# Optimization experiments

Measured on AMD Instinct MI355X. Metric: run time of the kernel, lower is better.

Reference implementation:

```python
import jax, jax.numpy as jnp
import numpy as np

N = 2048      # num_nodes (padded graph size)
D = 128       # node_embedding_dim
E = 8         # edge_embedding_dim (num learned edge-type channels)
ITERS = 8     # GGNN iterations (shared weights)


def setup_inputs() -> dict:
    key = jax.random.key(0)
    ks = jax.random.split(key, 8)
    s = 1.0 / np.sqrt(D)
    return {
        "node_embeddings": jax.random.normal(ks[0], (N, D), jnp.float32),
        # dense edge tensor; scaled by 1/N so the sum-over-senders message
        # aggregation stays O(1) in magnitude (real graphs are sparse)
        "edge_embeddings": jax.random.uniform(ks[1], (N, N, E), jnp.float32) / N,
        "W_msg": jax.random.normal(ks[2], (E, D, D), jnp.float32) * s,
        "b_msg": jnp.zeros((D,), jnp.float32),
        "Wi": jax.random.normal(ks[3], (D, 3 * D), jnp.float32) * s,
        "Wh": jax.random.normal(ks[4], (D, 3 * D), jnp.float32) * s,
        "b_gru": jnp.zeros((3 * D,), jnp.float32),
        "A_readout": jax.random.normal(ks[5], (D, D), jnp.float32) * s,
    }


def reference(node_embeddings, edge_embeddings, W_msg, b_msg, Wi, Wh, b_gru, A_readout):
    """GGNN steps (LinearMessagePassing + GRU update, weights shared via scan)
    followed by pairwise bilinear edge readout -> [N, N] logits."""

    def step(h, _):
        # per-edge-type linear transform of sender embeddings: [N, E, D]
        per_edge = jnp.einsum('sd,edh->seh', h, W_msg)
        # aggregate over senders weighted by dense edge tensor: [N, D]
        messages = jnp.einsum('ste,seh->th', edge_embeddings, per_edge) + b_msg
        # gated recurrent (GRU) update: state = node embeddings, input = messages
        gi = messages @ Wi + b_gru            # [N, 3D]
        gh = h @ Wh                           # [N, 3D]
        i_r, i_z, i_n = jnp.split(gi, 3, axis=-1)
        h_r, h_z, h_n = jnp.split(gh, 3, axis=-1)
        r = jax.nn.sigmoid(i_r + h_r)
        z = jax.nn.sigmoid(i_z + h_z)
        n = jnp.tanh(i_n + r * h_n)
        h_new = (1.0 - z) * n + z * h
        return h_new, None

    h, _ = jax.lax.scan(step, node_embeddings, None, length=ITERS)
    # bilinear pairwise readout -> weighted adjacency logits [N, N]
    logits = jnp.einsum('id,de,je->ij', h, A_readout, h)
    return logits
```

## Files before the change

### kernel.cpp

```cpp
#include <hip/hip_runtime.h>
#include <math.h>
#include <stdint.h>

#define Nn 2048
#define Dd 128
#define Ee 8
#define NIT 8
#define KT (Nn*Ee)
#define KSPLIT 32

typedef __bf16 bf16;
typedef __attribute__((ext_vector_type(8))) __bf16 bf16x8;
typedef __attribute__((ext_vector_type(4))) __bf16 bf16x4;
typedef __attribute__((ext_vector_type(4))) float f32x4;
typedef __attribute__((ext_vector_type(16))) float f32x16;

__device__ __forceinline__ f32x4 mfma16(bf16x8 a, bf16x8 b, f32x4 c){
    return __builtin_amdgcn_mfma_f32_16x16x32_bf16(a, b, c, 0, 0, 0);
}
__device__ __forceinline__ f32x16 mfma32(bf16x8 a, bf16x8 b, f32x16 c){
    return __builtin_amdgcn_mfma_f32_32x32x16_bf16(a, b, c, 0, 0, 0);
}
__device__ __forceinline__ void g2lds16(const void* g, void* l){
    __builtin_amdgcn_global_load_lds((const uint32_t*)g, (uint32_t*)l, 16, 0, 0);
}

__global__ __launch_bounds__(256) void k_prep(
    const float* __restrict__ node, const float* __restrict__ Wmsg,
    const float* __restrict__ Wi,   const float* __restrict__ Wh,
    const float* __restrict__ Ar,
    float* __restrict__ h32, bf16* __restrict__ hb,
    bf16* __restrict__ WmT, bf16* __restrict__ WiT, bf16* __restrict__ WhT,
    bf16* __restrict__ ArT)
{
    int tid = blockIdx.x*256 + threadIdx.x;
    int stride = gridDim.x*256;
    for (int i = tid; i < Nn*Dd; i += stride){
        float v = node[i]; h32[i] = v; hb[i] = (bf16)v;
    }
    for (int i = tid; i < Ee*Dd*Dd; i += stride){
        int e = i >> 14; int r = i & 16383; int h = r >> 7; int d = r & 127;
        WmT[i] = (bf16)Wmsg[e*Dd*Dd + d*Dd + h];
    }
    for (int i = tid; i < 384*Dd; i += stride){
        int j = i >> 7; int d = i & 127;
        WiT[i] = (bf16)Wi[d*384 + j];
        WhT[i] = (bf16)Wh[d*384 + j];
    }
    for (int i = tid; i < Dd*Dd; i += stride){
        int h = i >> 7; int d = i & 127;
        ArT[i] = (bf16)Ar[d*Dd + h];
    }
}

__global__ __launch_bounds__(256) void k_per_edge(
    const bf16* __restrict__ hb, const bf16* __restrict__ WmT,
    bf16* __restrict__ Pt)
{
    __shared__ bf16 Blds[Ee][16][Dd+8];
    const int s0 = blockIdx.x * 64;
    const int h0 = blockIdx.y * 16;
    const int tid = threadIdx.x;
    for (int i = 0; i < 8; i++){
        int idx = tid + i*256;
        int e = idx >> 8, row = (idx >> 4) & 15, c = idx & 15;
        *(bf16x8*)&Blds[e][row][c*8] =
            *(const bf16x8*)&WmT[e*Dd*Dd + (h0+row)*Dd + c*8];
    }
    __syncthreads();
    const int lane = tid & 63, wave = tid >> 6;
    const int quad = lane >> 4, l16 = lane & 15;
    const int srow = s0 + wave*16 + l16;
    f32x4 acc[Ee];
    for (int e = 0; e < Ee; e++) acc[e] = (f32x4){0.f,0.f,0.f,0.f};
    for (int kk = 0; kk < 4; kk++){
        int k0 = kk*32 + quad*8;
        bf16x8 a = *(const bf16x8*)&hb[srow*Dd + k0];
        for (int e = 0; e < Ee; e++){
            bf16x8 b = *(const bf16x8*)&Blds[e][l16][k0];
            acc[e] = mfma16(a, b, acc[e]);
        }
    }
    const int h = h0 + l16;
    for (int r = 0; r < 4; r++){
        int s = s0 + wave*16 + quad*4 + r;
        bf16x8 po;
        for (int e = 0; e < Ee; e++) po[e] = (bf16)acc[e][r];
        *(bf16x8*)&Pt[((size_t)s*Dd + h)*Ee] = po;
    }
}

template<int FIRST>
__global__ __launch_bounds__(256) void k_msg_gemm(
    const float* __restrict__ edge_f, bf16* __restrict__ edge_bf,
    const bf16* __restrict__ Pt, bf16* __restrict__ msgP)
{
    __shared__ __align__(16) char ldsb[65536];
    const int flat = blockIdx.y*32 + blockIdx.x;
    const int kgroup = (flat & 7)*4 + ((flat >> 3) & 3);
    const int tgroup = flat >> 5;
    const int t0 = tgroup * 128;
    const int sblk = kgroup * 64;
    const int tid = threadIdx.x;
    const int lane = tid & 63, wave = tid >> 6;
    const int half = lane >> 5, l31 = lane & 31;
    const int trow = t0 + wave*32 + l31;
    const char* Ptb = (const char*)Pt;

    f32x16 acc[4];
    #pragma unroll
    for (int nt = 0; nt < 4; nt++)
        for (int i = 0; i < 16; i++) acc[nt][i] = 0.f;

    bf16x8 A0[8], A1[8];

#define STAGE(ch_) do{                                                         \
    const char* _src = Ptb + (size_t)(sblk + (ch_)*16)*2048                    \
                           + wave*1024 + lane*16;                              \
    char* _dst = ldsb + ((ch_)&1)*32768 + wave*1024;                           \
    _Pragma("unroll")                                                          \
    for (int j = 0; j < 8; j++)                                                \
        g2lds16(_src + j*4096, _dst + j*4096);                                 \
}while(0)

#define PREF(AD_, ch_) do{                                                     \
    int _sc = sblk + (ch_)*16 + half;                                          \
    _Pragma("unroll")                                                          \
    for (int ks = 0; ks < 8; ks++){                                            \
        size_t _off = (size_t)(_sc + ks*2)*16384 + trow*8;                     \
        if (FIRST){                                                            \
            f32x4 _v0 = *(const f32x4*)&edge_f[_off];                          \
            f32x4 _v1 = *(const f32x4*)&edge_f[_off+4];                        \
            bf16x8 _o;                                                         \
            for (int _j = 0; _j < 4; _j++){                                    \
                _o[_j] = (bf16)_v0[_j]; _o[_j+4] = (bf16)_v1[_j];              \
            }                                                                  \
            AD_[ks] = _o;                                                      \
            *(bf16x8*)&edge_bf[_off] = _o;                                     \
        } else {                                                               \
            AD_[ks] = *(const bf16x8*)&edge_bf[_off];                          \
        }                                                                      \
    }                                                                          \
}while(0)

#define COMPUTE(AD_, ch_) do{                                                  \
    const bf16* _bt = (const bf16*)(ldsb + ((ch_)&1)*32768);                   \
    _Pragma("unroll")                                                          \
    for (int ks = 0; ks < 8; ks++){                                            \
        const bf16* _bp = _bt + (ks*2 + half)*1024 + l31*8;                    \
        acc[0] = mfma32(AD_[ks], *(const bf16x8*)(_bp      ), acc[0]);         \
        acc[1] = mfma32(AD_[ks], *(const bf16x8*)(_bp + 256), acc[1]);         \
        acc[2] = mfma32(AD_[ks], *(const bf16x8*)(_bp + 512), acc[2]);         \
        acc[3] = mfma32(AD_[ks], *(const bf16x8*)(_bp + 768), acc[3]);         \
    }                                                                          \
}while(0)

    STAGE(0); PREF(A0, 0);
    asm volatile("s_waitcnt vmcnt(0)" ::: "memory");
    __syncthreads();
    #pragma unroll
    for (int cc = 0; cc < 2; cc++){
        const int ch = cc*2;
        STAGE(ch+1); PREF(A1, ch+1);
        COMPUTE(A0, ch);
        asm volatile("s_waitcnt vmcnt(0)" ::: "memory");
        __syncthreads();
        if (ch+2 < 4){ STAGE(ch+2); PREF(A0, ch+2); }
        COMPUTE(A1, ch+1);
        if (ch+2 < 4){
            asm volatile("s_waitcnt vmcnt(0)" ::: "memory");
            __syncthreads();
        }
    }
#undef STAGE
#undef PREF
#undef COMPUTE

    bf16* dst = msgP + (size_t)kgroup*(Nn*Dd);
    #pragma unroll
    for (int nt = 0; nt < 4; nt++){
        int h = nt*32 + l31;
        #pragma unroll
        for (int r = 0; r < 16; r++){
            int row = (r&3) + 8*(r>>2) + 4*half;
            dst[(size_t)(t0 + wave*32 + row)*Dd + h] = (bf16)acc[nt][r];
        }
    }
}

__global__ __launch_bounds__(256) void k_msg_reduce(
    const bf16* __restrict__ msgP, const float* __restrict__ bmsg,
    bf16* __restrict__ msgb)
{
    const int base = (blockIdx.x*256 + threadIdx.x)*4;
    const int d0 = base & (Dd-1);
    f32x4 s = *(const f32x4*)&bmsg[d0];
    #pragma unroll
    for (int p = 0; p < KSPLIT; p++){
        bf16x4 v = *(const bf16x4*)&msgP[(size_t)p*Nn*Dd + base];
        #pragma unroll
        for (int j = 0; j < 4; j++) s[j] += (float)v[j];
    }
    bf16x4 o;
    #pragma unroll
    for (int j = 0; j < 4; j++) o[j] = (bf16)s[j];
    *(bf16x4*)&msgb[base] = o;
}

__global__ __launch_bounds__(256) void k_gru(
    const bf16* __restrict__ msgb, const bf16* __restrict__ WiT,
    const bf16* __restrict__ WhT, const float* __restrict__ bgru,
    float* __restrict__ h32, bf16* __restrict__ hb)
{
    __shared__ __align__(16) bf16 stage[384][40];
    __shared__ float Gs[16][384];
    __shared__ float Ghn[16][128];

    const int t0 = blockIdx.x * 16;
    const int tid = threadIdx.x;
    const int lane = tid & 63, wave = tid >> 6;
    const int quad = lane >> 4, l16 = lane & 15;

    f32x4 accA[6], accB[6];
    for (int i = 0; i < 6; i++){ accA[i] = (f32x4){0.f,0.f,0.f,0.f}; accB[i] = (f32x4){0.f,0.f,0.f,0.f}; }

    for (int mat = 0; mat < 2; mat++){
        const bf16* WT = mat == 0 ? WiT : WhT;
        for (int kc = 0; kc < 4; kc++){
            for (int i = 0; i < 6; i++){
                int idx = tid + i*256; int row = idx >> 2, c = idx & 3;
                *(bf16x8*)&stage[row][c*8] = *(const bf16x8*)&WT[row*Dd + kc*32 + c*8];
            }
            __syncthreads();
            int k0 = kc*32 + quad*8;
            bf16x8 a;
            if (mat == 0) a = *(const bf16x8*)&msgb[(t0 + l16)*Dd + k0];
            else          a = *(const bf16x8*)&hb  [(t0 + l16)*Dd + k0];
            for (int tt = 0; tt < 6; tt++){
                int T = wave*6 + tt;
                bf16x8 b = *(const bf16x8*)&stage[T*16 + l16][quad*8];
                if (mat == 0 || T < 16) accA[tt] = mfma16(a, b, accA[tt]);
                else                    accB[tt] = mfma16(a, b, accB[tt]);
            }
            __syncthreads();
        }
    }
    for (int tt = 0; tt < 6; tt++){
        int T = wave*6 + tt;
        int j = T*16 + l16;
        for (int r = 0; r < 4; r++){
            int m = quad*4 + r;
            Gs[m][j] = accA[tt][r];
            if (T >= 16) Ghn[m][j - 256] = accB[tt][r];
        }
    }
    __syncthreads();
    for (int i = 0; i < 8; i++){
        int cell = tid + i*256;
        int m = cell >> 7, jd = cell & 127;
        int t = t0 + m;
        float xr = Gs[m][jd]       + bgru[jd];
        float xz = Gs[m][jd + 128] + bgru[jd + 128];
        float xn = Gs[m][jd + 256] + bgru[jd + 256];
        float r = 1.f / (1.f + expf(-xr));
        float z = 1.f / (1.f + expf(-xz));
        float n = tanhf(xn + r * Ghn[m][jd]);
        float ho = h32[t*Dd + jd];
        float hnew = (1.f - z) * n + z * ho;
        h32[t*Dd + jd] = hnew;
        hb [t*Dd + jd] = (bf16)hnew;
    }
}

__global__ __launch_bounds__(256) void k_read1(
    const bf16* __restrict__ hb, const bf16* __restrict__ ArT, bf16* __restrict__ t1)
{
    __shared__ bf16 Blds[Dd][Dd+8];
    const int s0 = blockIdx.x * 64;
    const int tid = threadIdx.x;
    for (int i = 0; i < 8; i++){
        int idx = tid + i*256; int row = idx >> 4, c = idx & 15;
        *(bf16x8*)&Blds[row][c*8] = *(const bf16x8*)&ArT[row*Dd + c*8];
    }
    __syncthreads();
    const int lane = tid & 63, wave = tid >> 6;
    const int quad = lane >> 4, l16 = lane & 15;
    const int srow = s0 + wave*16 + l16;
    f32x4 acc[8];
    for (int nt = 0; nt < 8; nt++) acc[nt] = (f32x4){0.f,0.f,0.f,0.f};
    for (int kk = 0; kk < 4; kk++){
        int k0 = kk*32 + quad*8;
        bf16x8 a = *(const bf16x8*)&hb[srow*Dd + k0];
        for (int nt = 0; nt < 8; nt++){
            bf16x8 b = *(const bf16x8*)&Blds[nt*16 + l16][k0];
            acc[nt] = mfma16(a, b, acc[nt]);
        }
    }
    for (int nt = 0; nt < 8; nt++){
        int h = nt*16 + l16;
        for (int r = 0; r < 4; r++){
            int s = s0 + wave*16 + quad*4 + r;
            t1[s*Dd + h] = (bf16)acc[nt][r];
        }
    }
}

__global__ __launch_bounds__(256) void k_read2(
    const bf16* __restrict__ t1, const bf16* __restrict__ hb, float* __restrict__ out)
{
    const int i0 = blockIdx.x * 64, j0 = blockIdx.y * 128;
    const int tid = threadIdx.x;
    const int lane = tid & 63, wave = tid >> 6;
    const int quad = lane >> 4, l16 = lane & 15;
    const int irow = i0 + wave*16 + l16;
    f32x4 acc[8];
    for (int nt = 0; nt < 8; nt++) acc[nt] = (f32x4){0.f,0.f,0.f,0.f};
    for (int kk = 0; kk < 4; kk++){
        int k0 = kk*32 + quad*8;
        bf16x8 a = *(const bf16x8*)&t1[irow*Dd + k0];
        for (int nt = 0; nt < 8; nt++){
            int j = j0 + nt*16 + l16;
            bf16x8 b = *(const bf16x8*)&hb[j*Dd + k0];
            acc[nt] = mfma16(a, b, acc[nt]);
        }
    }
    for (int nt = 0; nt < 8; nt++){
        int j = j0 + nt*16 + l16;
        for (int r = 0; r < 4; r++){
            int irw = i0 + wave*16 + quad*4 + r;
            out[(size_t)irw*Nn + j] = acc[nt][r];
        }
    }
}

extern "C" void kernel_launch(void* const* d_in, const int* in_sizes, int n_in,
                              void* d_out, int out_size, void* d_ws, size_t ws_size,
                              hipStream_t stream)
{
    const float* node = (const float*)d_in[0];
    const float* edge = (const float*)d_in[1];
    const float* Wmsg = (const float*)d_in[2];
    const float* bmsg = (const float*)d_in[3];
    const float* Wi   = (const float*)d_in[4];
    const float* Wh   = (const float*)d_in[5];
    const float* bgru = (const float*)d_in[6];
    const float* Ar   = (const float*)d_in[7];
    float* out = (float*)d_out;

    char* ws = (char*)d_ws;
    bf16*  edge_bf = (bf16*)ws;          ws += (size_t)Nn*Nn*Ee*2;
    bf16*  msgP = (bf16*)ws;             ws += (size_t)KSPLIT*Nn*Dd*2;
    bf16*  Pt  = (bf16*)ws;              ws += (size_t)Dd*KT*2;
    float* h32 = (float*)ws;             ws += (size_t)Nn*Dd*4;
    bf16*  hb  = (bf16*)ws;              ws += (size_t)Nn*Dd*2;
    bf16*  WmT = (bf16*)ws;              ws += (size_t)Ee*Dd*Dd*2;
    bf16*  WiT = (bf16*)ws;              ws += (size_t)384*Dd*2;
    bf16*  WhT = (bf16*)ws;              ws += (size_t)384*Dd*2;
    bf16*  ArT = (bf16*)ws;              ws += (size_t)Dd*Dd*2;
    bf16*  t1  = (bf16*)ws;              ws += (size_t)Nn*Dd*2;
    bf16*  msgb = t1;

    k_prep<<<dim3(256), 256, 0, stream>>>(node, Wmsg, Wi, Wh, Ar,
                                          h32, hb, WmT, WiT, WhT, ArT);
    for (int it = 0; it < NIT; it++){
        k_per_edge<<<dim3(32, 8), 256, 0, stream>>>(hb, WmT, Pt);
        if (it == 0)
            k_msg_gemm<1><<<dim3(32,16), 256, 0, stream>>>(edge, edge_bf, Pt, msgP);
        else
            k_msg_gemm<0><<<dim3(32,16), 256, 0, stream>>>(edge, edge_bf, Pt, msgP);
        k_msg_reduce<<<dim3(256), 256, 0, stream>>>(msgP, bmsg, msgb);
        k_gru<<<dim3(128), 256, 0, stream>>>(msgb, WiT, WhT, bgru, h32, hb);
    }
    k_read1<<<dim3(32),     256, 0, stream>>>(hb, ArT, t1);
    k_read2<<<dim3(32, 16), 256, 0, stream>>>(t1, hb, out);
}
```

Measured before the change: 561.0 us.

## Fuse message reduce and per-edge transform into GRU kernel; fuse readout GEMMs

```diff
diff --git a/kernel.cpp b/kernel.cpp
--- a/kernel.cpp
+++ b/kernel.cpp
@@ -188,38 +188,43 @@
     }
 }
 
-__global__ __launch_bounds__(256) void k_msg_reduce(
+__global__ __launch_bounds__(256) void k_gru2(
     const bf16* __restrict__ msgP, const float* __restrict__ bmsg,
-    bf16* __restrict__ msgb)
-{
-    const int base = (blockIdx.x*256 + threadIdx.x)*4;
-    const int d0 = base & (Dd-1);
-    f32x4 s = *(const f32x4*)&bmsg[d0];
-    #pragma unroll
-    for (int p = 0; p < KSPLIT; p++){
-        bf16x4 v = *(const bf16x4*)&msgP[(size_t)p*Nn*Dd + base];
-        #pragma unroll
-        for (int j = 0; j < 4; j++) s[j] += (float)v[j];
-    }
-    bf16x4 o;
-    #pragma unroll
-    for (int j = 0; j < 4; j++) o[j] = (bf16)s[j];
-    *(bf16x4*)&msgb[base] = o;
-}
-
-__global__ __launch_bounds__(256) void k_gru(
-    const bf16* __restrict__ msgb, const bf16* __restrict__ WiT,
-    const bf16* __restrict__ WhT, const float* __restrict__ bgru,
-    float* __restrict__ h32, bf16* __restrict__ hb)
+    const bf16* __restrict__ WiT,  const bf16* __restrict__ WhT,
+    const float* __restrict__ bgru, const bf16* __restrict__ WmT,
+    float* __restrict__ h32, bf16* __restrict__ hb, bf16* __restrict__ Pt)
 {
     __shared__ __align__(16) bf16 stage[384][40];
     __shared__ float Gs[16][384];
     __shared__ float Ghn[16][128];
+    __shared__ __align__(16) bf16 msg_b[16][136];
+    __shared__ __align__(16) bf16 hn_b[16][136];
 
     const int t0 = blockIdx.x * 16;
     const int tid = threadIdx.x;
     const int lane = tid & 63, wave = tid >> 6;
     const int quad = lane >> 4, l16 = lane & 15;
+
+    {
+        int m = tid >> 4;
+        int d0 = (tid & 15) * 8;
+        f32x4 s0 = *(const f32x4*)&bmsg[d0];
+        f32x4 s1 = *(const f32x4*)&bmsg[d0+4];
+        #pragma unroll
+        for (int p = 0; p < KSPLIT; p++){
+            bf16x8 v = *(const bf16x8*)&msgP[(size_t)p*Nn*Dd + (t0+m)*Dd + d0];
+            #pragma unroll
+            for (int j = 0; j < 4; j++){
+                s0[j] += (float)v[j];
+                s1[j] += (float)v[j+4];
+            }
+        }
+        bf16x8 o;
+        #pragma unroll
+        for (int j = 0; j < 4; j++){ o[j] = (bf16)s0[j]; o[j+4] = (bf16)s1[j]; }
+        *(bf16x8*)&msg_b[m][d0] = o;
+    }
+    __syncthreads();
 
     f32x4 accA[6], accB[6];
     for (int i = 0; i < 6; i++){ accA[i] = (f32x4){0.f,0.f,0.f,0.f}; accB[i] = (f32x4){0.f,0.f,0.f,0.f}; }
@@ -234,8 +239,8 @@
             __syncthreads();
             int k0 = kc*32 + quad*8;
             bf16x8 a;
-            if (mat == 0) a = *(const bf16x8*)&msgb[(t0 + l16)*Dd + k0];
-            else          a = *(const bf16x8*)&hb  [(t0 + l16)*Dd + k0];
+            if (mat == 0) a = *(const bf16x8*)&msg_b[l16][k0];
+            else          a = *(const bf16x8*)&hb[(t0 + l16)*Dd + k0];
             for (int tt = 0; tt < 6; tt++){
                 int T = wave*6 + tt;
                 bf16x8 b = *(const bf16x8*)&stage[T*16 + l16][quad*8];
@@ -255,6 +260,7 @@
         }
     }
     __syncthreads();
+
     for (int i = 0; i < 8; i++){
         int cell = tid + i*256;
         int m = cell >> 7, jd = cell & 127;
@@ -268,15 +274,52 @@
         float ho = h32[t*Dd + jd];
         float hnew = (1.f - z) * n + z * ho;
         h32[t*Dd + jd] = hnew;
-        hb [t*Dd + jd] = (bf16)hnew;
-    }
-}
-
-__global__ __launch_bounds__(256) void k_read1(
-    const bf16* __restrict__ hb, const bf16* __restrict__ ArT, bf16* __restrict__ t1)
+        bf16 hv = (bf16)hnew;
+        hb [t*Dd + jd] = hv;
+        hn_b[m][jd] = hv;
+    }
+    __syncthreads();
+
+    {
+        f32x4 accP[2][8];
+        #pragma unroll
+        for (int i = 0; i < 2; i++)
+            for (int e = 0; e < 8; e++) accP[i][e] = (f32x4){0.f,0.f,0.f,0.f};
+        #pragma unroll
+        for (int kk = 0; kk < 4; kk++){
+            int k0 = kk*32 + quad*8;
+            bf16x8 a = *(const bf16x8*)&hn_b[l16][k0];
+            #pragma unroll
+            for (int i = 0; i < 2; i++){
+                int th = wave*2 + i;
+                #pragma unroll
+                for (int e = 0; e < 8; e++){
+                    bf16x8 b = *(const bf16x8*)&WmT[e*Dd*Dd + (th*16 + l16)*Dd + k0];
+                    accP[i][e] = mfma16(a, b, accP[i][e]);
+                }
+            }
+        }
+        #pragma unroll
+        for (int i = 0; i < 2; i++){
+            int h = (wave*2 + i)*16 + l16;
+            #pragma unroll
+            for (int r = 0; r < 4; r++){
+                int s = quad*4 + r;
+                bf16x8 po;
+                for (int e = 0; e < 8; e++) po[e] = (bf16)accP[i][e][r];
+                *(bf16x8*)&Pt[((size_t)(t0 + s)*Dd + h)*Ee] = po;
+            }
+        }
+    }
+}
+
+__global__ __launch_bounds__(256) void k_read2f(
+    const bf16* __restrict__ hb, const bf16* __restrict__ ArT,
+    float* __restrict__ out)
 {
     __shared__ bf16 Blds[Dd][Dd+8];
-    const int s0 = blockIdx.x * 64;
+    __shared__ bf16 t1s[64][136];
+    const int i0 = blockIdx.x * 64, j0 = blockIdx.y * 128;
     const int tid = threadIdx.x;
     for (int i = 0; i < 8; i++){
         int idx = tid + i*256; int row = idx >> 4, c = idx & 15;
@@ -285,39 +328,34 @@
     __syncthreads();
     const int lane = tid & 63, wave = tid >> 6;
     const int quad = lane >> 4, l16 = lane & 15;
-    const int srow = s0 + wave*16 + l16;
+
+    {
+        const int srow = i0 + wave*16 + l16;
+        f32x4 acc1[8];
+        for (int nt = 0; nt < 8; nt++) acc1[nt] = (f32x4){0.f,0.f,0.f,0.f};
+        for (int kk = 0; kk < 4; kk++){
+            int k0 = kk*32 + quad*8;
+            bf16x8 a = *(const bf16x8*)&hb[srow*Dd + k0];
+            for (int nt = 0; nt < 8; nt++){
+                bf16x8 b = *(const bf16x8*)&Blds[nt*16 + l16][k0];
+                acc1[nt] = mfma16(a, b, acc1[nt]);
+            }
+        }
+        for (int nt = 0; nt < 8; nt++){
+            int h = nt*16 + l16;
+            for (int r = 0; r < 4; r++){
+                int rr = wave*16 + quad*4 + r;
+                t1s[rr][h] = (bf16)acc1[nt][r];
+            }
+        }
+    }
+    __syncthreads();
+
     f32x4 acc[8];
     for (int nt = 0; nt < 8; nt++) acc[nt] = (f32x4){0.f,0.f,0.f,0.f};
     for (int kk = 0; kk < 4; kk++){
         int k0 = kk*32 + quad*8;
-        bf16x8 a = *(const bf16x8*)&hb[srow*Dd + k0];
-        for (int nt = 0; nt < 8; nt++){
-            bf16x8 b = *(const bf16x8*)&Blds[nt*16 + l16][k0];
-            acc[nt] = mfma16(a, b, acc[nt]);
-        }
-    }
-    for (int nt = 0; nt < 8; nt++){
-        int h = nt*16 + l16;
-        for (int r = 0; r < 4; r++){
-            int s = s0 + wave*16 + quad*4 + r;
-            t1[s*Dd + h] = (bf16)acc[nt][r];
-        }
-    }
-}
-
-__global__ __launch_bounds__(256) void k_read2(
-    const bf16* __restrict__ t1, const bf16* __restrict__ hb, float* __restrict__ out)
-{
-    const int i0 = blockIdx.x * 64, j0 = blockIdx.y * 128;
-    const int tid = threadIdx.x;
-    const int lane = tid & 63, wave = tid >> 6;
-    const int quad = lane >> 4, l16 = lane & 15;
-    const int irow = i0 + wave*16 + l16;
-    f32x4 acc[8];
-    for (int nt = 0; nt < 8; nt++) acc[nt] = (f32x4){0.f,0.f,0.f,0.f};
-    for (int kk = 0; kk < 4; kk++){
-        int k0 = kk*32 + quad*8;
-        bf16x8 a = *(const bf16x8*)&t1[irow*Dd + k0];
+        bf16x8 a = *(const bf16x8*)&t1s[wave*16 + l16][k0];
         for (int nt = 0; nt < 8; nt++){
             int j = j0 + nt*16 + l16;
             bf16x8 b = *(const bf16x8*)&hb[j*Dd + k0];
@@ -357,20 +395,17 @@
     bf16*  WiT = (bf16*)ws;              ws += (size_t)384*Dd*2;
     bf16*  WhT = (bf16*)ws;              ws += (size_t)384*Dd*2;
     bf16*  ArT = (bf16*)ws;              ws += (size_t)Dd*Dd*2;
-    bf16*  t1  = (bf16*)ws;              ws += (size_t)Nn*Dd*2;
-    bf16*  msgb = t1;
 
     k_prep<<<dim3(256), 256, 0, stream>>>(node, Wmsg, Wi, Wh, Ar,
                                           h32, hb, WmT, WiT, WhT, ArT);
+    k_per_edge<<<dim3(32, 8), 256, 0, stream>>>(hb, WmT, Pt);
     for (int it = 0; it < NIT; it++){
-        k_per_edge<<<dim3(32, 8), 256, 0, stream>>>(hb, WmT, Pt);
         if (it == 0)
             k_msg_gemm<1><<<dim3(32,16), 256, 0, stream>>>(edge, edge_bf, Pt, msgP);
         else
             k_msg_gemm<0><<<dim3(32,16), 256, 0, stream>>>(edge, edge_bf, Pt, msgP);
-        k_msg_reduce<<<dim3(256), 256, 0, stream>>>(msgP, bmsg, msgb);
-        k_gru<<<dim3(128), 256, 0, stream>>>(msgb, WiT, WhT, bgru, h32, hb);
-    }
-    k_read1<<<dim3(32),     256, 0, stream>>>(hb, ArT, t1);
-    k_read2<<<dim3(32, 16), 256, 0, stream>>>(t1, hb, out);
-}
+        k_gru2<<<dim3(128), 256, 0, stream>>>(msgP, bmsg, WiT, WhT, bgru,
+                                              WmT, h32, hb, Pt);
+    }
+    k_read2f<<<dim3(32, 16), 256, 0, stream>>>(hb, ArT, out);
+}
```

After: 581.7 us. 1.04x slower.

## Fuse split-K message reduction into GRU kernel with 8-row tiles

Applied to the files above, without the earlier changes.

```diff
diff --git a/kernel.cpp b/kernel.cpp
--- a/kernel.cpp
+++ b/kernel.cpp
@@ -188,83 +188,87 @@
     }
 }
 
-__global__ __launch_bounds__(256) void k_msg_reduce(
+__global__ __launch_bounds__(256) void k_gru3(
     const bf16* __restrict__ msgP, const float* __restrict__ bmsg,
-    bf16* __restrict__ msgb)
-{
-    const int base = (blockIdx.x*256 + threadIdx.x)*4;
-    const int d0 = base & (Dd-1);
-    f32x4 s = *(const f32x4*)&bmsg[d0];
-    #pragma unroll
-    for (int p = 0; p < KSPLIT; p++){
-        bf16x4 v = *(const bf16x4*)&msgP[(size_t)p*Nn*Dd + base];
-        #pragma unroll
-        for (int j = 0; j < 4; j++) s[j] += (float)v[j];
-    }
-    bf16x4 o;
-    #pragma unroll
-    for (int j = 0; j < 4; j++) o[j] = (bf16)s[j];
-    *(bf16x4*)&msgb[base] = o;
-}
-
-__global__ __launch_bounds__(256) void k_gru(
-    const bf16* __restrict__ msgb, const bf16* __restrict__ WiT,
-    const bf16* __restrict__ WhT, const float* __restrict__ bgru,
+    const bf16* __restrict__ WiT, const bf16* __restrict__ WhT,
+    const float* __restrict__ bgru,
     float* __restrict__ h32, bf16* __restrict__ hb)
 {
-    __shared__ __align__(16) bf16 stage[384][40];
-    __shared__ float Gs[16][384];
-    __shared__ float Ghn[16][128];
-
-    const int t0 = blockIdx.x * 16;
+    __shared__ __align__(16) bf16 msg_b[16][136];
+    __shared__ __align__(16) bf16 h_b[16][136];
+    __shared__ float Gs [8][388];
+    __shared__ float Ghf[8][388];
+
+    const int t0 = blockIdx.x * 8;
     const int tid = threadIdx.x;
     const int lane = tid & 63, wave = tid >> 6;
     const int quad = lane >> 4, l16 = lane & 15;
 
-    f32x4 accA[6], accB[6];
-    for (int i = 0; i < 6; i++){ accA[i] = (f32x4){0.f,0.f,0.f,0.f}; accB[i] = (f32x4){0.f,0.f,0.f,0.f}; }
-
-    for (int mat = 0; mat < 2; mat++){
-        const bf16* WT = mat == 0 ? WiT : WhT;
-        for (int kc = 0; kc < 4; kc++){
-            for (int i = 0; i < 6; i++){
-                int idx = tid + i*256; int row = idx >> 2, c = idx & 3;
-                *(bf16x8*)&stage[row][c*8] = *(const bf16x8*)&WT[row*Dd + kc*32 + c*8];
-            }
-            __syncthreads();
-            int k0 = kc*32 + quad*8;
-            bf16x8 a;
-            if (mat == 0) a = *(const bf16x8*)&msgb[(t0 + l16)*Dd + k0];
-            else          a = *(const bf16x8*)&hb  [(t0 + l16)*Dd + k0];
-            for (int tt = 0; tt < 6; tt++){
-                int T = wave*6 + tt;
-                bf16x8 b = *(const bf16x8*)&stage[T*16 + l16][quad*8];
-                if (mat == 0 || T < 16) accA[tt] = mfma16(a, b, accA[tt]);
-                else                    accB[tt] = mfma16(a, b, accB[tt]);
-            }
-            __syncthreads();
-        }
-    }
-    for (int tt = 0; tt < 6; tt++){
-        int T = wave*6 + tt;
-        int j = T*16 + l16;
+    for (int i = tid; i < 8*136; i += 256){
+        (&msg_b[8][0])[i] = (bf16)0.f;
+        (&h_b [8][0])[i] = (bf16)0.f;
+    }
+
+    {
+        int m = tid >> 5;
+        int d0 = (tid & 31) * 4;
+        f32x4 s = *(const f32x4*)&bmsg[d0];
+        #pragma unroll
+        for (int p = 0; p < KSPLIT; p++){
+            bf16x4 v = *(const bf16x4*)&msgP[(size_t)p*Nn*Dd + (t0+m)*Dd + d0];
+            #pragma unroll
+            for (int j = 0; j < 4; j++) s[j] += (float)v[j];
+        }
+        bf16x4 o;
+        #pragma unroll
+        for (int j = 0; j < 4; j++) o[j] = (bf16)s[j];
+        *(bf16x4*)&msg_b[m][d0] = o;
+        *(bf16x4*)&h_b[m][d0] = *(const bf16x4*)&hb[(t0+m)*Dd + d0];
+    }
+    __syncthreads();
+
+    f32x4 accA[12];
+    #pragma unroll
+    for (int i = 0; i < 12; i++) accA[i] = (f32x4){0.f,0.f,0.f,0.f};
+    #pragma unroll
+    for (int kc = 0; kc < 4; kc++){
+        int k0 = kc*32 + quad*8;
+        bf16x8 aGi = *(const bf16x8*)&msg_b[l16][k0];
+        bf16x8 aGh = *(const bf16x8*)&h_b[l16][k0];
+        #pragma unroll
+        for (int i = 0; i < 12; i++){
+            int T = wave*12 + i;
+            int isGi = T < 24;
+            int jt = isGi ? T : T - 24;
+            const bf16* WT = isGi ? WiT : WhT;
+            bf16x8 b = *(const bf16x8*)&WT[(jt*16 + l16)*Dd + k0];
+            accA[i] = mfma16(isGi ? aGi : aGh, b, accA[i]);
+        }
+    }
+    #pragma unroll
+    for (int i = 0; i < 12; i++){
+        int T = wave*12 + i;
+        int jt = T < 24 ? T : T - 24;
+        float* G = T < 24 ? &Gs[0][0] : &Ghf[0][0];
+        #pragma unroll
         for (int r = 0; r < 4; r++){
-            int m = quad*4 + r;
-            Gs[m][j] = accA[tt][r];
-            if (T >= 16) Ghn[m][j - 256] = accB[tt][r];
-        }
-    }
-    __syncthreads();
-    for (int i = 0; i < 8; i++){
+            int row = quad*4 + r;
+            if (row < 8) G[row*388 + jt*16 + l16] = accA[i][r];
+        }
+    }
+    __syncthreads();
+
+    #pragma unroll
+    for (int i = 0; i < 4; i++){
         int cell = tid + i*256;
         int m = cell >> 7, jd = cell & 127;
         int t = t0 + m;
-        float xr = Gs[m][jd]       + bgru[jd];
-        float xz = Gs[m][jd + 128] + bgru[jd + 128];
-        float xn = Gs[m][jd + 256] + bgru[jd + 256];
+        float xr = Gs[m][jd]       + Ghf[m][jd]       + bgru[jd];
+        float xz = Gs[m][128 + jd] + Ghf[m][128 + jd] + bgru[128 + jd];
+        float xn = Gs[m][256 + jd] + bgru[256 + jd];
         float r = 1.f / (1.f + expf(-xr));
         float z = 1.f / (1.f + expf(-xz));
-        float n = tanhf(xn + r * Ghn[m][jd]);
+        float n = tanhf(xn + r * Ghf[m][256 + jd]);
         float ho = h32[t*Dd + jd];
         float hnew = (1.f - z) * n + z * ho;
         h32[t*Dd + jd] = hnew;
@@ -358,7 +362,6 @@
     bf16*  WhT = (bf16*)ws;              ws += (size_t)384*Dd*2;
     bf16*  ArT = (bf16*)ws;              ws += (size_t)Dd*Dd*2;
     bf16*  t1  = (bf16*)ws;              ws += (size_t)Nn*Dd*2;
-    bf16*  msgb = t1;
 
     k_prep<<<dim3(256), 256, 0, stream>>>(node, Wmsg, Wi, Wh, Ar,
                                           h32, hb, WmT, WiT, WhT, ArT);
@@ -368,8 +371,7 @@
             k_msg_gemm<1><<<dim3(32,16), 256, 0, stream>>>(edge, edge_bf, Pt, msgP);
         else
             k_msg_gemm<0><<<dim3(32,16), 256, 0, stream>>>(edge, edge_bf, Pt, msgP);
-        k_msg_reduce<<<dim3(256), 256, 0, stream>>>(msgP, bmsg, msgb);
-        k_gru<<<dim3(128), 256, 0, stream>>>(msgb, WiT, WhT, bgru, h32, hb);
+        k_gru3<<<dim3(256), 256, 0, stream>>>(msgP, bmsg, WiT, WhT, bgru, h32, hb);
     }
     k_read1<<<dim3(32),     256, 0, stream>>>(hb, ArT, t1);
     k_read2<<<dim3(32, 16), 256, 0, stream>>>(t1, hb, out);
```

New measurement: 525.6 us. -6.3%, faster.
